# Kernel optimization log

Hardware: AMD Instinct MI355X
Metric: run time of the kernel (lower is better)

## Reference

```python
import jax, jax.numpy as jnp
import numpy as np

N_NODES = 40000
N_PAIRS = 640000
F = 128


def setup_inputs() -> dict:
    key = jax.random.key(0)
    k1, k2, k3, k4, k5, k6 = jax.random.split(key, 6)
    x = jax.random.normal(k1, (N_NODES, F), dtype=jnp.float32)
    w_ij = jax.random.normal(k2, (N_PAIRS, F), dtype=jnp.float32)
    idx_i = jax.random.randint(k3, (N_PAIRS,), 0, N_NODES)
    idx_j = jax.random.randint(k4, (N_PAIRS,), 0, N_NODES)
    # Dense(use_bias=False) kernels, shape (in_features, out_features)
    Wq = jax.random.normal(k5, (F, F), dtype=jnp.float32) / np.sqrt(F)
    Wk = jax.random.normal(k6, (F, F), dtype=jnp.float32) / np.sqrt(F)
    return {"x": x, "w_ij": w_ij, "idx_i": idx_i, "idx_j": idx_j, "Wq": Wq, "Wk": Wk}


def reference(x, w_ij, idx_i, idx_j, Wq, Wk):
    # Dense projections on node embeddings: (n, F)
    q = x @ Wq
    k = x @ Wk
    # Gather per-edge, elementwise multiply with filter, reduce over F
    # out: (n_pairs,)
    inv_sqrt_f = 1.0 / jnp.sqrt(jnp.asarray(x.shape[-1], dtype=x.dtype))
    return (q[idx_i] * w_ij * k[idx_j]).sum(axis=-1) * inv_sqrt_f
```

## Files before the change

### kernel.cpp

```cpp
#include <hip/hip_runtime.h>

#define F 128
#define NODES_PER_CHUNK 32
#define CHUNKS_PER_BLOCK 5
#define PAIRS_PER_BLOCK 32

static __device__ __forceinline__ unsigned short f2bf(float f) {
    unsigned int u = __float_as_uint(f);
    u += 0x7FFFu + ((u >> 16) & 1u);
    return (unsigned short)(u >> 16);
}
static __device__ __forceinline__ float bf2f(unsigned short h) {
    return __uint_as_float(((unsigned int)h) << 16);
}

__global__ __launch_bounds__(256) void proj_kernel(
    const float* __restrict__ x,
    const float* __restrict__ Wq,
    const float* __restrict__ Wk,
    unsigned short* __restrict__ q,
    unsigned short* __restrict__ k)
{
    __shared__ float lds_w[F * F];
    __shared__ float lds_x[NODES_PER_CHUNK * F];

    const int t   = threadIdx.x;
    const int isK = blockIdx.y;
    const float* __restrict__ W      = isK ? Wk : Wq;
    unsigned short* __restrict__ outp = isK ? k  : q;

    {
        const float4* w4 = (const float4*)W;
        float4* l4 = (float4*)lds_w;
        #pragma unroll
        for (int i = 0; i < 16; ++i) l4[i * 256 + t] = w4[i * 256 + t];
    }

    const int cg = t & 31;
    const int rg = t >> 5;

    for (int c = 0; c < CHUNKS_PER_BLOCK; ++c) {
        const int r0 = (blockIdx.x * CHUNKS_PER_BLOCK + c) * NODES_PER_CHUNK;

        __syncthreads();
        {
            const float4* x4 = (const float4*)(x + (size_t)r0 * F);
            float4* l4 = (float4*)lds_x;
            #pragma unroll
            for (int i = 0; i < 4; ++i) l4[i * 256 + t] = x4[i * 256 + t];
        }
        __syncthreads();

        float acc[4][4] = {};
        #pragma unroll 4
        for (int f4 = 0; f4 < 32; ++f4) {
            float4 xv[4];
            #pragma unroll
            for (int r = 0; r < 4; ++r)
                xv[r] = *(const float4*)&lds_x[(4 * rg + r) * F + 4 * f4];
            #pragma unroll
            for (int j = 0; j < 4; ++j) {
                const float4 wv = *(const float4*)&lds_w[(4 * f4 + j) * F + 4 * cg];
                #pragma unroll
                for (int r = 0; r < 4; ++r) {
                    const float xs = ((const float*)&xv[r])[j];
                    acc[r][0] += xs * wv.x;
                    acc[r][1] += xs * wv.y;
                    acc[r][2] += xs * wv.z;
                    acc[r][3] += xs * wv.w;
                }
            }
        }

        #pragma unroll
        for (int r = 0; r < 4; ++r) {
            ushort4 v;
            v.x = f2bf(acc[r][0]);
            v.y = f2bf(acc[r][1]);
            v.z = f2bf(acc[r][2]);
            v.w = f2bf(acc[r][3]);
            *(ushort4*)&outp[(size_t)(r0 + 4 * rg + r) * F + 4 * cg] = v;
        }
    }
}

__global__ __launch_bounds__(256) void edge_kernel(
    const float* __restrict__ w_ij,
    const int*   __restrict__ idx_i,
    const int*   __restrict__ idx_j,
    const unsigned short* __restrict__ q,
    const unsigned short* __restrict__ k,
    float* __restrict__ out)
{
    __shared__ int sidx[2 * PAIRS_PER_BLOCK];

    const int p0 = blockIdx.x * PAIRS_PER_BLOCK;
    const int t  = threadIdx.x;

    if (t < 64) {
        sidx[t] = (t < 32) ? idx_i[p0 + t] : idx_j[p0 + t - 32];
    }
    __syncthreads();

    const int hw = t >> 5;
    const int l  = t & 31;

    float4  wv[4];
    ushort4 qv[4], kv[4];
    #pragma unroll
    for (int u = 0; u < 4; ++u) {
        const int pp = hw * 4 + u;
        const int i = sidx[pp];
        const int j = sidx[PAIRS_PER_BLOCK + pp];
        wv[u] = *(const float4*)&w_ij[(size_t)(p0 + pp) * F + 4 * l];
        qv[u] = *(const ushort4*)&q[(size_t)i * F + 4 * l];
        kv[u] = *(const ushort4*)&k[(size_t)j * F + 4 * l];
    }

    #pragma unroll
    for (int u = 0; u < 4; ++u) {
        float s = bf2f(qv[u].x) * bf2f(kv[u].x) * wv[u].x
                + bf2f(qv[u].y) * bf2f(kv[u].y) * wv[u].y
                + bf2f(qv[u].z) * bf2f(kv[u].z) * wv[u].z
                + bf2f(qv[u].w) * bf2f(kv[u].w) * wv[u].w;
        s += __shfl_xor(s, 16);
        s += __shfl_xor(s, 8);
        s += __shfl_xor(s, 4);
        s += __shfl_xor(s, 2);
        s += __shfl_xor(s, 1);
        if (l == 0) out[p0 + hw * 4 + u] = s * 0.088388347648318447f;
    }
}

extern "C" void kernel_launch(void* const* d_in, const int* in_sizes, int n_in,
                              void* d_out, int out_size, void* d_ws, size_t ws_size,
                              hipStream_t stream) {
    const float* x     = (const float*)d_in[0];
    const float* w_ij  = (const float*)d_in[1];
    const int*   idx_i = (const int*)d_in[2];
    const int*   idx_j = (const int*)d_in[3];
    const float* Wq    = (const float*)d_in[4];
    const float* Wk    = (const float*)d_in[5];
    float* out = (float*)d_out;

    const int n_nodes = in_sizes[0] / F;
    const int n_pairs = in_sizes[2];

    unsigned short* q = (unsigned short*)d_ws;
    unsigned short* k = q + (size_t)n_nodes * F;

    dim3 g1(n_nodes / (NODES_PER_CHUNK * CHUNKS_PER_BLOCK), 2);
    proj_kernel<<<g1, 256, 0, stream>>>(x, Wq, Wk, q, k);

    int g2 = n_pairs / PAIRS_PER_BLOCK;
    edge_kernel<<<g2, 256, 0, stream>>>(w_ij, idx_i, idx_j, q, k, out);
}
```

Baseline: 484.9 us.

## Compute node projections with split-bf16 MFMA and pre-swizzled weight layout

```diff
diff --git a/kernel.cpp b/kernel.cpp
--- a/kernel.cpp
+++ b/kernel.cpp
@@ -1,9 +1,10 @@
 #include <hip/hip_runtime.h>
 
 #define F 128
-#define NODES_PER_CHUNK 32
-#define CHUNKS_PER_BLOCK 5
 #define PAIRS_PER_BLOCK 32
+
+typedef __attribute__((ext_vector_type(8))) short bf16x8;
+typedef __attribute__((ext_vector_type(4))) float f32x4;
 
 static __device__ __forceinline__ unsigned short f2bf(float f) {
     unsigned int u = __float_as_uint(f);
@@ -14,74 +15,111 @@
     return __uint_as_float(((unsigned int)h) << 16);
 }
 
-__global__ __launch_bounds__(256) void proj_kernel(
-    const float* __restrict__ x,
+__global__ __launch_bounds__(256) void prep_w(
     const float* __restrict__ Wq,
     const float* __restrict__ Wk,
+    unsigned short* __restrict__ wt)
+{
+    const int gid = blockIdx.x * 256 + threadIdx.x;
+    const int sel = gid >> 14;
+    const int e   = gid & 16383;
+    const int kk  = e >> 7;
+    const int n   = e & 127;
+    const float v = (sel ? Wk : Wq)[e];
+    const unsigned short hi = f2bf(v);
+    const unsigned short lo = f2bf(v - bf2f(hi));
+    const int idx = n * F + (kk ^ ((n & 7) << 3));
+    unsigned short* base = wt + sel * 32768;
+    base[idx]         = hi;
+    base[16384 + idx] = lo;
+}
+
+__global__ __launch_bounds__(256) void proj_mfma(
+    const float* __restrict__ x,
+    const unsigned short* __restrict__ wt,
     unsigned short* __restrict__ q,
     unsigned short* __restrict__ k)
 {
-    __shared__ float lds_w[F * F];
-    __shared__ float lds_x[NODES_PER_CHUNK * F];
+    __shared__ unsigned short lds_w[2 * 16384];
 
     const int t   = threadIdx.x;
     const int isK = blockIdx.y;
-    const float* __restrict__ W      = isK ? Wk : Wq;
-    unsigned short* __restrict__ outp = isK ? k  : q;
+    const unsigned short* __restrict__ wsrc = wt + (size_t)isK * 32768;
+    unsigned short* __restrict__ outp = isK ? k : q;
 
     {
-        const float4* w4 = (const float4*)W;
-        float4* l4 = (float4*)lds_w;
+        const int4* src = (const int4*)wsrc;
+        int4* dst = (int4*)lds_w;
         #pragma unroll
-        for (int i = 0; i < 16; ++i) l4[i * 256 + t] = w4[i * 256 + t];
+        for (int i = 0; i < 16; ++i) dst[i * 256 + t] = src[i * 256 + t];
+    }
+    __syncthreads();
+
+    const int w     = t >> 6;
+    const int l     = t & 63;
+    const int l15   = l & 15;
+    const int lg    = l >> 4;
+    const int rbase = blockIdx.x * 64 + (w >> 1) * 32;
+    const int cbase = (w & 1) * 64;
+
+    f32x4 acc[2][4] = {};
+
+    #pragma unroll
+    for (int ks = 0; ks < 4; ++ks) {
+        bf16x8 ahi[2], alo[2];
+        #pragma unroll
+        for (int rt = 0; rt < 2; ++rt) {
+            const float* xp = x + (size_t)(rbase + rt * 16 + l15) * F + ks * 32 + lg * 8;
+            const float4 v0 = *(const float4*)xp;
+            const float4 v1 = *(const float4*)(xp + 4);
+            const float vv[8] = {v0.x, v0.y, v0.z, v0.w, v1.x, v1.y, v1.z, v1.w};
+            #pragma unroll
+            for (int e = 0; e < 8; ++e) {
+                const unsigned short h = f2bf(vv[e]);
+                ahi[rt][e] = (short)h;
+                alo[rt][e] = (short)f2bf(vv[e] - bf2f(h));
+            }
+        }
+        bf16x8 bhi[4], blo[4];
+        #pragma unroll
+        for (int nt = 0; nt < 4; ++nt) {
+            const int n   = cbase + nt * 16 + l15;
+            const int kk  = ks * 32 + lg * 8;
+            const int idx = n * F + (kk ^ ((n & 7) << 3));
+            bhi[nt] = *(const bf16x8*)&lds_w[idx];
+            blo[nt] = *(const bf16x8*)&lds_w[16384 + idx];
+        }
+        #pragma unroll
+        for (int rt = 0; rt < 2; ++rt)
+            #pragma unroll
+            for (int nt = 0; nt < 4; ++nt)
+                acc[rt][nt] = __builtin_amdgcn_mfma_f32_16x16x32_bf16(
+                    ahi[rt], bhi[nt], acc[rt][nt], 0, 0, 0);
+        #pragma unroll
+        for (int rt = 0; rt < 2; ++rt)
+            #pragma unroll
+            for (int nt = 0; nt < 4; ++nt)
+                acc[rt][nt] = __builtin_amdgcn_mfma_f32_16x16x32_bf16(
+                    ahi[rt], blo[nt], acc[rt][nt], 0, 0, 0);
+        #pragma unroll
+        for (int rt = 0; rt < 2; ++rt)
+            #pragma unroll
+            for (int nt = 0; nt < 4; ++nt)
+                acc[rt][nt] = __builtin_amdgcn_mfma_f32_16x16x32_bf16(
+                    alo[rt], bhi[nt], acc[rt][nt], 0, 0, 0);
     }
 
-    const int cg = t & 31;
-    const int rg = t >> 5;
-
-    for (int c = 0; c < CHUNKS_PER_BLOCK; ++c) {
-        const int r0 = (blockIdx.x * CHUNKS_PER_BLOCK + c) * NODES_PER_CHUNK;
-
-        __syncthreads();
-        {
-            const float4* x4 = (const float4*)(x + (size_t)r0 * F);
-            float4* l4 = (float4*)lds_x;
+    #pragma unroll
+    for (int rt = 0; rt < 2; ++rt)
+        #pragma unroll
+        for (int nt = 0; nt < 4; ++nt) {
+            const int col = cbase + nt * 16 + l15;
             #pragma unroll
-            for (int i = 0; i < 4; ++i) l4[i * 256 + t] = x4[i * 256 + t];
-        }
-        __syncthreads();
-
-        float acc[4][4] = {};
-        #pragma unroll 4
-        for (int f4 = 0; f4 < 32; ++f4) {
-            float4 xv[4];
-            #pragma unroll
-            for (int r = 0; r < 4; ++r)
-                xv[r] = *(const float4*)&lds_x[(4 * rg + r) * F + 4 * f4];
-            #pragma unroll
-            for (int j = 0; j < 4; ++j) {
-                const float4 wv = *(const float4*)&lds_w[(4 * f4 + j) * F + 4 * cg];
-                #pragma unroll
-                for (int r = 0; r < 4; ++r) {
-                    const float xs = ((const float*)&xv[r])[j];
-                    acc[r][0] += xs * wv.x;
-                    acc[r][1] += xs * wv.y;
-                    acc[r][2] += xs * wv.z;
-                    acc[r][3] += xs * wv.w;
-                }
+            for (int r = 0; r < 4; ++r) {
+                const int row = rbase + rt * 16 + lg * 4 + r;
+                outp[(size_t)row * F + col] = f2bf(acc[rt][nt][r]);
             }
         }
-
-        #pragma unroll
-        for (int r = 0; r < 4; ++r) {
-            ushort4 v;
-            v.x = f2bf(acc[r][0]);
-            v.y = f2bf(acc[r][1]);
-            v.z = f2bf(acc[r][2]);
-            v.w = f2bf(acc[r][3]);
-            *(ushort4*)&outp[(size_t)(r0 + 4 * rg + r) * F + 4 * cg] = v;
-        }
-    }
 }
 
 __global__ __launch_bounds__(256) void edge_kernel(
@@ -146,11 +184,14 @@
     const int n_nodes = in_sizes[0] / F;
     const int n_pairs = in_sizes[2];
 
-    unsigned short* q = (unsigned short*)d_ws;
-    unsigned short* k = q + (size_t)n_nodes * F;
+    unsigned short* q  = (unsigned short*)d_ws;
+    unsigned short* k  = q + (size_t)n_nodes * F;
+    unsigned short* wt = k + (size_t)n_nodes * F;
 
-    dim3 g1(n_nodes / (NODES_PER_CHUNK * CHUNKS_PER_BLOCK), 2);
-    proj_kernel<<<g1, 256, 0, stream>>>(x, Wq, Wk, q, k);
+    prep_w<<<128, 256, 0, stream>>>(Wq, Wk, wt);
+
+    dim3 g1(n_nodes / 64, 2);
+    proj_mfma<<<g1, 256, 0, stream>>>(x, wt, q, k);
 
     int g2 = n_pairs / PAIRS_PER_BLOCK;
     edge_kernel<<<g2, 256, 0, stream>>>(w_ij, idx_i, idx_j, q, k, out);
```

New measurement: 468.6 us. -3.4%, faster.
